# Optimization experiments

Measured on AMD Instinct MI355X. Metric: run time of the kernel, lower is better.

The kernel has to match this reference:

```python
import jax, jax.numpy as jnp
import numpy as np
import math

D_MODEL = 1024
N_HEADS = 16
D_HEAD = D_MODEL // N_HEADS

def setup_inputs() -> dict:
    key = jax.random.key(0)
    k1, k2, k3 = jax.random.split(key, 3)
    x = jax.random.normal(k1, (4, 2048, D_MODEL), dtype=jnp.float32)
    # torch Linear weights are [out, in]; kept in that layout, applied as x @ W.T
    s = 1.0 / math.sqrt(D_MODEL)
    W_qkv = jax.random.uniform(k2, (3 * D_MODEL, D_MODEL), jnp.float32, -s, s)
    W_proj = jax.random.uniform(k3, (D_MODEL, D_MODEL), jnp.float32, -s, s)
    return {"x": x, "W_qkv": W_qkv, "W_proj": W_proj}

def reference(x, W_qkv, W_proj):
    B, T, d = x.shape
    qkv = x @ W_qkv.T  # [B,T,3d]
    q, k, v = jnp.split(qkv, 3, axis=-1)
    def split(t):
        return t.reshape(B, T, N_HEADS, D_HEAD).transpose(0, 2, 1, 3)  # [B,H,T,Dh]
    q, k, v = split(q), split(k), split(v)
    scores = jnp.einsum('bhqd,bhkd->bhqk', q, k) / math.sqrt(D_HEAD)
    mask = jnp.tril(jnp.ones((T, T), dtype=bool))
    scores = jnp.where(mask, scores, -jnp.inf)
    attn = jax.nn.softmax(scores, axis=-1)
    out = jnp.einsum('bhqk,bhkd->bhqd', attn, v)  # [B,H,T,Dh]
    out = out.transpose(0, 2, 1, 3).reshape(B, T, d)
    return out @ W_proj.T
```

## Files before the change

### kernel.cpp

```cpp
#include <hip/hip_runtime.h>
#include <hip/hip_bf16.h>
#include <math.h>

typedef __attribute__((ext_vector_type(8))) short short8;
typedef __attribute__((ext_vector_type(4))) float f32x4;
typedef __attribute__((ext_vector_type(16))) float f32x16;
typedef __attribute__((ext_vector_type(2))) unsigned uint2v;
typedef __attribute__((ext_vector_type(4))) unsigned uint4v;

#define B_  4
#define T_  2048
#define DM  1024
#define NH  16
#define DH  64
#define BH  (B_*NH)
#define M_  (B_*T_)

#define QSCALE 0.18033688011112042f

static __device__ __forceinline__ short f2bf(float f) {
  unsigned u = __float_as_uint(f);
  unsigned r = (u + 0x7fff + ((u >> 16) & 1)) >> 16;
  return (short)r;
}

static __device__ __forceinline__ float bf2f(short s) {
  return __uint_as_float(((unsigned)(unsigned short)s) << 16);
}

static __device__ __forceinline__ unsigned cvtpk(float lo, float hi) {
  unsigned r;
  asm("v_cvt_pk_bf16_f32 %0, %1, %2" : "=v"(r) : "v"(lo), "v"(hi));
  return r;
}

static __device__ __forceinline__ float expasm(float x) {
  float r;
  asm("v_exp_f32 %0, %1" : "=v"(r) : "v"(x));
  return r;
}

static __device__ __forceinline__ void gload_lds16(const void* g, void* l) {
  __builtin_amdgcn_global_load_lds((const __attribute__((address_space(1))) void*)g,
                                   (__attribute__((address_space(3))) void*)l, 16, 0, 0);
}

__global__ void k_cvt3(const float4* __restrict__ x, const float4* __restrict__ wq,
                       const float4* __restrict__ wp, ushort4* __restrict__ ox,
                       ushort4* __restrict__ oq, ushort4* __restrict__ op) {
  const int n1 = M_ * DM / 4, n2 = 3 * DM * DM / 4, n3 = DM * DM / 4;
  int i = blockIdx.x * 256 + threadIdx.x;
  const float4* src;
  ushort4* dst;
  int j = i;
  if (i < n1) { src = x; dst = ox; }
  else if (i < n1 + n2) { src = wq; dst = oq; j = i - n1; }
  else if (i < n1 + n2 + n3) { src = wp; dst = op; j = i - n1 - n2; }
  else return;
  float4 v = src[j];
  ushort4 o;
  o.x = (ushort)f2bf(v.x); o.y = (ushort)f2bf(v.y);
  o.z = (ushort)f2bf(v.z); o.w = (ushort)f2bf(v.w);
  dst[j] = o;
}

#define GEMM_STAGE(SRCA, SRCB, dA, dB, m0_, n0_, k0_)                          \
  {                                                                            \
    _Pragma("unroll")                                                          \
    for (int i = 0; i < 4; ++i) {                                              \
      int lin = i * 256 + tid;                                                 \
      int row = lin >> 3, pseg = lin & 7;                                      \
      int gseg = pseg ^ (row & 7);                                             \
      gload_lds16(&SRCA[(size_t)((m0_) + row) * DM + (k0_) + gseg * 8],        \
                  &(dA)[lin * 8]);                                             \
    }                                                                          \
    _Pragma("unroll")                                                          \
    for (int i = 0; i < 4; ++i) {                                              \
      int lin = i * 256 + tid;                                                 \
      int row = lin >> 3, pseg = lin & 7;                                      \
      int gseg = pseg ^ (row & 7);                                             \
      gload_lds16(&SRCB[(size_t)((n0_) + row) * DM + (k0_) + gseg * 8],        \
                  &(dB)[lin * 8]);                                             \
    }                                                                          \
  }

#define GEMM_COMPUTE(pA, pB)                                                   \
  {                                                                            \
    _Pragma("unroll")                                                          \
    for (int kk = 0; kk < 2; ++kk) {                                           \
      short8 aF[4], bF[4];                                                     \
      _Pragma("unroll")                                                        \
      for (int m = 0; m < 4; ++m)                                              \
        aF[m] = *(const short8*)&(pA)[(wr * 64 + m * 16 + fr) * 64 +           \
                                      (((kk * 4 + fq) ^ (fr & 7)) * 8)];       \
      _Pragma("unroll")                                                        \
      for (int n = 0; n < 4; ++n)                                              \
        bF[n] = *(const short8*)&(pB)[(wc * 64 + n * 16 + fr) * 64 +           \
                                      (((kk * 4 + fq) ^ (fr & 7)) * 8)];       \
      __builtin_amdgcn_s_setprio(1);                                           \
      _Pragma("unroll")                                                        \
      for (int m = 0; m < 4; ++m)                                              \
        _Pragma("unroll")                                                      \
        for (int n = 0; n < 4; ++n)                                            \
          acc[m][n] = __builtin_amdgcn_mfma_f32_16x16x32_bf16(aF[m], bF[n],    \
                                                              acc[m][n], 0, 0, 0); \
      __builtin_amdgcn_s_setprio(0);                                           \
    }                                                                          \
  }

#define GEMM_KLOOP(SRCA, SRCB, m0_, n0_)                                       \
  GEMM_STAGE(SRCA, SRCB, sA0, sB0, m0_, n0_, 0);                               \
  {                                                                            \
    _Pragma("unroll 1")                                                        \
    for (int t = 0; t < 16; ++t) {                                             \
      short* pA = (t & 1) ? sA1 : sA0;                                         \
      short* pB = (t & 1) ? sB1 : sB0;                                         \
      if (t < 15) {                                                            \
        short* nA = (t & 1) ? sA0 : sA1;                                       \
        short* nB = (t & 1) ? sB0 : sB1;                                       \
        GEMM_STAGE(SRCA, SRCB, nA, nB, m0_, n0_, (t + 1) * 64);                \
        asm volatile("s_waitcnt vmcnt(8)" ::: "memory");                       \
      } else {                                                                 \
        asm volatile("s_waitcnt vmcnt(0)" ::: "memory");                       \
      }                                                                        \
      __builtin_amdgcn_s_barrier();                                            \
      __builtin_amdgcn_sched_barrier(0);                                       \
      GEMM_COMPUTE(pA, pB);                                                    \
      asm volatile("" ::: "memory");                                           \
      __builtin_amdgcn_s_barrier();                                            \
    }                                                                          \
  }

__global__ __launch_bounds__(256, 2) void k_gemm_qkv(
    const short* __restrict__ A,
    const short* __restrict__ W,
    short* __restrict__ Qb, short* __restrict__ Kb, short* __restrict__ Vtb) {
  const int tid = threadIdx.x;
  const int w = tid >> 6, l = tid & 63;
  const int wr = w >> 1, wc = w & 1;
  const int fq = l >> 4, fr = l & 15;
  const int m0 = blockIdx.x * 128;
  const int n0 = blockIdx.y * 128;

  __shared__ short lds[32768];
  short* sA0 = lds;
  short* sA1 = lds + 8192;
  short* sB0 = lds + 16384;
  short* sB1 = lds + 24576;

  f32x4 acc[4][4] = {};
  GEMM_KLOOP(A, W, m0, n0);
  __syncthreads();

  short* sE = lds;
  const int part = n0 >> 10;
  const int b = m0 >> 11, tloc = m0 & 2047;

  if (part < 2) {
    const float sc = part ? 1.0f : QSCALE;
#pragma unroll
    for (int m = 0; m < 4; ++m)
#pragma unroll
      for (int n = 0; n < 4; ++n)
#pragma unroll
        for (int j = 0; j < 4; ++j)
          sE[(wr * 64 + m * 16 + fq * 4 + j) * 136 + wc * 64 + n * 16 + fr] =
              f2bf(acc[m][n][j] * sc);
    __syncthreads();
    short* dst = part ? Kb : Qb;
    const int h0 = (n0 & 1023) >> 6;
#pragma unroll
    for (int v = 0; v < 8; ++v) {
      int vid = v * 256 + tid;
      int row = vid >> 4, seg = vid & 15;
      short8 val = *(const short8*)&sE[row * 136 + seg * 8];
      int h = h0 + (seg >> 3), dh0 = (seg & 7) * 8;
      *(short8*)&dst[(((size_t)(b * NH + h) * T_ + tloc + row)) * DH + dh0] = val;
    }
  } else {
#pragma unroll
    for (int m = 0; m < 4; ++m)
#pragma unroll
      for (int n = 0; n < 4; ++n) {
        uint2v pk;
        pk[0] = cvtpk(acc[m][n][0], acc[m][n][1]);
        pk[1] = cvtpk(acc[m][n][2], acc[m][n][3]);
        *(uint2v*)&sE[(wc * 64 + n * 16 + fr) * 136 + wr * 64 + m * 16 + fq * 4] = pk;
      }
    __syncthreads();
    const int h0 = (n0 & 1023) >> 6;
#pragma unroll
    for (int v = 0; v < 8; ++v) {
      int vid = v * 256 + tid;
      int col = vid >> 4, seg = vid & 15;
      short8 val = *(const short8*)&sE[col * 136 + seg * 8];
      int h = h0 + (col >> 6), dh = col & 63;
      *(short8*)&Vtb[(((size_t)(b * NH + h) * DH + dh)) * T_ + tloc + seg * 8] = val;
    }
  }
}

__global__ __launch_bounds__(256, 2) void k_gemm_proj(
    const short* __restrict__ A,
    const short* __restrict__ W,
    float* __restrict__ C) {
  const int tid = threadIdx.x;
  const int w = tid >> 6, l = tid & 63;
  const int wr = w >> 1, wc = w & 1;
  const int fq = l >> 4, fr = l & 15;
  const int m0 = blockIdx.x * 128;
  const int n0 = blockIdx.y * 128;

  __shared__ short lds[32768];
  short* sA0 = lds;
  short* sA1 = lds + 8192;
  short* sB0 = lds + 16384;
  short* sB1 = lds + 24576;

  f32x4 acc[4][4] = {};
  GEMM_KLOOP(A, W, m0, n0);

#pragma unroll
  for (int m = 0; m < 4; ++m) {
    int row0 = m0 + wr * 64 + m * 16 + fq * 4;
#pragma unroll
    for (int n = 0; n < 4; ++n) {
      int col = n0 + wc * 64 + n * 16 + fr;
#pragma unroll
      for (int j = 0; j < 4; ++j)
        C[(size_t)(row0 + j) * DM + col] = acc[m][n][j];
    }
  }
}

__global__ __launch_bounds__(256, 2) void k_attn9(
    const short* __restrict__ Qb,
    const short* __restrict__ Kb,
    const short* __restrict__ Vtb,
    short* __restrict__ Ob,
    unsigned* __restrict__ Pbuf,
    float* __restrict__ Lbuf) {
  const int tid = threadIdx.x;
  const int w = tid >> 6, l = tid & 63;
  const int lq = l & 31, hi = l >> 5;
  const int id = blockIdx.x;
  const int x = id >> 6;
  const int u = (x < 4) ? (2 * x) : (2 * (x - 4) + 1);
  const int bh = id & 63;
  const int qtA = 7 - (u >> 1);
  const int b = bh >> 4, h = bh & 15;

  __shared__ short lds[16384];
  short* sK = lds;
  short* sVt = lds + 8192;

  auto STAGE = [&](int buf, int kt) {
#pragma unroll
    for (int i = 0; i < 2; ++i) {
      int lin = i * 256 + tid;
      int row = lin >> 3, pseg = lin & 7;
      int gseg = pseg ^ (row & 7);
      gload_lds16(&Kb[((size_t)bh * T_ + kt * 64 + row) * DH + gseg * 8],
                  &sK[buf * 4096 + lin * 8]);
    }
#pragma unroll
    for (int i = 0; i < 2; ++i) {
      int lin = i * 256 + tid;
      int row = lin >> 3, pseg = lin & 7;
      int gseg = pseg ^ (row & 7);
      gload_lds16(&Vtb[((size_t)bh * DH + row) * T_ + kt * 64 + gseg * 8],
                  &sVt[buf * 4096 + lin * 8]);
    }
  };

  auto SMAX = [&](int kt, int q0s, f32x16& sa, f32x16& sb, float& lsum, short8 (&pb)[4]) {
    if (kt * 64 + 63 > q0s) {
      const int qg = q0s + lq;
#pragma unroll
      for (int r = 0; r < 16; ++r) {
        int kg0 = kt * 64 + (r & 3) + 8 * (r >> 2) + 4 * hi;
        if (kg0 > qg) sa[r] = -1e30f;
        if (kg0 + 32 > qg) sb[r] = -1e30f;
      }
    }
#pragma unroll
    for (int r = 0; r < 16; ++r) {
      sa[r] = expasm(sa[r]);
      sb[r] = expasm(sb[r]);
    }
    {
      float t[8];
#pragma unroll
      for (int i = 0; i < 8; ++i)
        t[i] = (sa[2 * i] + sa[2 * i + 1]) + (sb[2 * i] + sb[2 * i + 1]);
      float u0 = (t[0] + t[1]) + (t[2] + t[3]);
      float u1 = (t[4] + t[5]) + (t[6] + t[7]);
      lsum += u0 + u1;
    }
#pragma unroll
    for (int st = 0; st < 2; ++st) {
      const f32x16& P = st ? sb : sa;
      unsigned x0 = cvtpk(P[0], P[1]);
      unsigned x1 = cvtpk(P[2], P[3]);
      unsigned y0 = cvtpk(P[4], P[5]);
      unsigned y1 = cvtpk(P[6], P[7]);
      uint2v r0 = __builtin_amdgcn_permlane32_swap(x0, y0, false, false);
      uint2v r1 = __builtin_amdgcn_permlane32_swap(x1, y1, false, false);
      unsigned x2 = cvtpk(P[8], P[9]);
      unsigned x3 = cvtpk(P[10], P[11]);
      unsigned y2 = cvtpk(P[12], P[13]);
      unsigned y3 = cvtpk(P[14], P[15]);
      uint2v r2 = __builtin_amdgcn_permlane32_swap(x2, y2, false, false);
      uint2v r3 = __builtin_amdgcn_permlane32_swap(x3, y3, false, false);
      uint4v ta, tb;
      ta[0] = r0[0]; ta[1] = r1[0]; ta[2] = r0[1]; ta[3] = r1[1];
      tb[0] = r2[0]; tb[1] = r3[0]; tb[2] = r2[1]; tb[3] = r3[1];
      pb[st * 2 + 0] = __builtin_bit_cast(short8, ta);
      pb[st * 2 + 1] = __builtin_bit_cast(short8, tb);
    }
  };

  auto RUN_SEG = [&](int qt, int k0, int k1, int ppid) {
    const int q00 = qt * 256 + w * 32;
    const int q01 = q00 + 128;
    short8 qf0[4], qf1[4];
#pragma unroll
    for (int c = 0; c < 4; ++c) {
      qf0[c] = *(const short8*)&Qb[((size_t)bh * T_ + q00 + lq) * DH + c * 16 + hi * 8];
      qf1[c] = *(const short8*)&Qb[((size_t)bh * T_ + q01 + lq) * DH + c * 16 + hi * 8];
    }
    float ls0 = 0.f, ls1 = 0.f;
    f32x16 oa0[2] = {}, oa1[2] = {};

    auto CSUB2 = [&](int kt, const int koff) {
      const bool do0 = (kt * 64 <= q00 + 31);
      const bool do1 = (kt * 64 <= q01 + 31);
      f32x16 s0a = {}, s0b = {}, s1a = {}, s1b = {};
      __builtin_amdgcn_s_setprio(1);
#pragma unroll
      for (int st = 0; st < 2; ++st) {
        short8 kf[4];
#pragma unroll
        for (int c = 0; c < 4; ++c)
          kf[c] = *(const short8*)&sK[koff + (st * 32 + lq) * 64 +
                                      (((2 * c + hi) ^ (lq & 7)) * 8)];
        f32x16& d0 = st ? s0b : s0a;
        f32x16& d1 = st ? s1b : s1a;
#pragma unroll
        for (int c = 0; c < 4; ++c) {
          if (do0) d0 = __builtin_amdgcn_mfma_f32_32x32x16_bf16(kf[c], qf0[c], d0, 0, 0, 0);
          if (do1) d1 = __builtin_amdgcn_mfma_f32_32x32x16_bf16(kf[c], qf1[c], d1, 0, 0, 0);
        }
      }
      __builtin_amdgcn_s_setprio(0);

      short8 pb0[4], pb1[4];
      if (do0) SMAX(kt, q00, s0a, s0b, ls0, pb0);
      if (do1) SMAX(kt, q01, s1a, s1b, ls1, pb1);

      __builtin_amdgcn_s_setprio(1);
#pragma unroll
      for (int dt = 0; dt < 2; ++dt) {
        short8 vf[4];
#pragma unroll
        for (int c = 0; c < 4; ++c)
          vf[c] = *(const short8*)&sVt[koff + (dt * 32 + lq) * 64 +
                                       (((2 * c + hi) ^ (lq & 7)) * 8)];
#pragma unroll
        for (int c = 0; c < 4; ++c) {
          if (do0) oa0[dt] = __builtin_amdgcn_mfma_f32_32x32x16_bf16(vf[c], pb0[c], oa0[dt], 0, 0, 0);
          if (do1) oa1[dt] = __builtin_amdgcn_mfma_f32_32x32x16_bf16(vf[c], pb1[c], oa1[dt], 0, 0, 0);
        }
      }
      __builtin_amdgcn_s_setprio(0);
    };

    STAGE(0, k0);
    int t = k0;
    while (true) {
      if (t + 1 < k1) {
        STAGE(1, t + 1);
        asm volatile("s_waitcnt vmcnt(4)" ::: "memory");
      } else {
        asm volatile("s_waitcnt vmcnt(0)" ::: "memory");
      }
      __builtin_amdgcn_s_barrier();
      __builtin_amdgcn_sched_barrier(0);
      CSUB2(t, 0);
      __builtin_amdgcn_s_barrier();
      if (++t == k1) break;

      if (t + 1 < k1) {
        STAGE(0, t + 1);
        asm volatile("s_waitcnt vmcnt(4)" ::: "memory");
      } else {
        asm volatile("s_waitcnt vmcnt(0)" ::: "memory");
      }
      __builtin_amdgcn_s_barrier();
      __builtin_amdgcn_sched_barrier(0);
      CSUB2(t, 4096);
      __builtin_amdgcn_s_barrier();
      if (++t == k1) break;
    }

    ls0 += __shfl_xor(ls0, 32);
    ls1 += __shfl_xor(ls1, 32);

    if (ppid >= 0) {
      unsigned* Pb = Pbuf + (size_t)ppid * 8192;
#pragma unroll
      for (int sub = 0; sub < 2; ++sub) {
        const f32x16* OA = sub ? oa1 : oa0;
#pragma unroll
        for (int dt = 0; dt < 2; ++dt)
#pragma unroll
          for (int p = 0; p < 8; ++p)
            Pb[(((sub * 4 + w) * 2 + dt) * 8 + p) * 64 + l] =
                cvtpk(OA[dt][2 * p], OA[dt][2 * p + 1]);
      }
      if (hi == 0) {
        Lbuf[ppid * 256 + (0 * 4 + w) * 32 + lq] = ls0;
        Lbuf[ppid * 256 + (1 * 4 + w) * 32 + lq] = ls1;
      }
    } else {
      __syncthreads();
      short* sO = lds + w * 2304;
      const int qr = l >> 1, hf = l & 1;
      {
        float inv = 1.0f / ls0;
#pragma unroll
        for (int dt = 0; dt < 2; ++dt)
#pragma unroll
          for (int r = 0; r < 16; r += 2) {
            int dl = dt * 32 + (r & 3) + 8 * (r >> 2) + 4 * hi;
            *(unsigned*)&sO[lq * 72 + dl] = cvtpk(oa0[dt][r] * inv, oa0[dt][r + 1] * inv);
          }
        asm volatile("s_waitcnt lgkmcnt(0)" ::: "memory");
        __builtin_amdgcn_sched_barrier(0);
        const int tg = qt * 256 + w * 32 + qr;
#pragma unroll
        for (int ss = 0; ss < 4; ++ss) {
          short8 v = *(const short8*)&sO[qr * 72 + hf * 32 + ss * 8];
          *(short8*)&Ob[((size_t)(b * T_) + tg) * DM + h * 64 + hf * 32 + ss * 8] = v;
        }
        asm volatile("s_waitcnt lgkmcnt(0)" ::: "memory");
        __builtin_amdgcn_sched_barrier(0);
      }
      {
        float inv = 1.0f / ls1;
#pragma unroll
        for (int dt = 0; dt < 2; ++dt)
#pragma unroll
          for (int r = 0; r < 16; r += 2) {
            int dl = dt * 32 + (r & 3) + 8 * (r >> 2) + 4 * hi;
            *(unsigned*)&sO[lq * 72 + dl] = cvtpk(oa1[dt][r] * inv, oa1[dt][r + 1] * inv);
          }
        asm volatile("s_waitcnt lgkmcnt(0)" ::: "memory");
        __builtin_amdgcn_sched_barrier(0);
        const int tg = qt * 256 + 128 + w * 32 + qr;
#pragma unroll
        for (int ss = 0; ss < 4; ++ss) {
          short8 v = *(const short8*)&sO[qr * 72 + hf * 32 + ss * 8];
          *(short8*)&Ob[((size_t)(b * T_) + tg) * DM + h * 64 + hf * 32 + ss * 8] = v;
        }
      }
    }
  };

  if ((u & 1) == 0) {
    RUN_SEG(qtA, 0, 18, (bh * 4 + (qtA - 4)) * 2 + 0);
  } else {
    RUN_SEG(qtA, 18, 4 * qtA + 4, (bh * 4 + (qtA - 4)) * 2 + 1);
    const int qtB = u >> 1;
    RUN_SEG(qtB, 0, 4 * qtB + 4, -1);
  }
}

__global__ __launch_bounds__(256) void k_merge(
    const unsigned* __restrict__ P, const float* __restrict__ L,
    short* __restrict__ Ob) {
  const int tid = threadIdx.x;
  const int w = tid >> 6, l = tid & 63;
  const int lq = l & 31, hi = l >> 5;
  const int sid = blockIdx.x;
  const int bh = sid & 63, qtm = sid >> 6;
  const int qt = 4 + qtm;
  const int b = bh >> 4, h = bh & 15;
  const int pid0 = (bh * 4 + qtm) * 2;
  const unsigned* P0 = P + (size_t)pid0 * 8192;
  const unsigned* P1 = P0 + 8192;

  __shared__ short sOm[9216];
  short* sO = sOm + w * 2304;
  const int qr = l >> 1, hf = l & 1;

#pragma unroll
  for (int sub = 0; sub < 2; ++sub) {
    float l0 = L[pid0 * 256 + (sub * 4 + w) * 32 + lq];
    float l1 = L[(pid0 + 1) * 256 + (sub * 4 + w) * 32 + lq];
    float inv = 1.0f / (l0 + l1);
#pragma unroll
    for (int dt = 0; dt < 2; ++dt)
#pragma unroll
      for (int p = 0; p < 8; ++p) {
        int idx = (((sub * 4 + w) * 2 + dt) * 8 + p) * 64 + l;
        unsigned u0 = P0[idx], u1 = P1[idx];
        float e0 = bf2f((short)(u0 & 0xffff)) + bf2f((short)(u1 & 0xffff));
        float e1 = bf2f((short)(u0 >> 16)) + bf2f((short)(u1 >> 16));
        int r = 2 * p;
        int dl = dt * 32 + (r & 3) + 8 * (r >> 2) + 4 * hi;
        *(unsigned*)&sO[lq * 72 + dl] = cvtpk(e0 * inv, e1 * inv);
      }
    asm volatile("s_waitcnt lgkmcnt(0)" ::: "memory");
    __builtin_amdgcn_sched_barrier(0);
    const int tg = qt * 256 + sub * 128 + w * 32 + qr;
#pragma unroll
    for (int ss = 0; ss < 4; ++ss) {
      short8 v = *(const short8*)&sO[qr * 72 + hf * 32 + ss * 8];
      *(short8*)&Ob[((size_t)(b * T_) + tg) * DM + h * 64 + hf * 32 + ss * 8] = v;
    }
    asm volatile("s_waitcnt lgkmcnt(0)" ::: "memory");
    __builtin_amdgcn_sched_barrier(0);
  }
}

extern "C" void kernel_launch(void* const* d_in, const int* in_sizes, int n_in,
                              void* d_out, int out_size, void* d_ws, size_t ws_size,
                              hipStream_t stream) {
  const float* x     = (const float*)d_in[0];
  const float* Wqkv  = (const float*)d_in[1];
  const float* Wproj = (const float*)d_in[2];
  float* out = (float*)d_out;

  short* ws = (short*)d_ws;
  short* xbf   = ws;
  short* wqkvb = xbf + (size_t)M_ * DM;
  short* wprjb = wqkvb + (size_t)3 * DM * DM;
  short* Qb    = wprjb + (size_t)DM * DM;
  short* Kb    = Qb + (size_t)BH * T_ * DH;
  short* Vtb   = Kb + (size_t)BH * T_ * DH;
  short* Ob    = Vtb + (size_t)BH * T_ * DH;
  unsigned* Pbuf = (unsigned*)xbf;
  float* Lbuf    = (float*)wqkvb;

  const int ncv = (M_ * DM + 3 * DM * DM + DM * DM) / 4;
  k_cvt3<<<(ncv + 255) / 256, 256, 0, stream>>>(
      (const float4*)x, (const float4*)Wqkv, (const float4*)Wproj,
      (ushort4*)xbf, (ushort4*)wqkvb, (ushort4*)wprjb);

  k_gemm_qkv<<<dim3(M_ / 128, 3 * DM / 128), 256, 0, stream>>>(xbf, wqkvb, Qb, Kb, Vtb);
  k_attn9<<<512, 256, 0, stream>>>(Qb, Kb, Vtb, Ob, Pbuf, Lbuf);
  k_merge<<<256, 256, 0, stream>>>(Pbuf, Lbuf, Ob);
  k_gemm_proj<<<dim3(M_ / 128, DM / 128), 256, 0, stream>>>(Ob, wprjb, out);
}
```

Measured before the change: 143.5 us.

## Restructure GEMMs to 256x128 tiles with 8 waves and triple-buffered split-phase loads

Both projection GEMMs move from 128x128 tiles with 4 waves and double buffering to 256x128 tiles with 8 waves (512 threads) and a three-slot LDS ring. Each 64-wide k step is split into two phases, and each phase issues an A or B prefetch for a later stage while computing from the current slot. The aim is better B-tile reuse and more load latency hidden behind MFMA work. In exchange, each block uses 144KB of LDS, so only one block fits per CU, the grid is halved, and the epilogue indexing changes. The V-transpose epilogue now uses a 264-element LDS stride.

```diff
diff --git a/kernel.cpp b/kernel.cpp
--- a/kernel.cpp
+++ b/kernel.cpp
@@ -64,74 +64,84 @@
   dst[j] = o;
 }
 
-#define GEMM_STAGE(SRCA, SRCB, dA, dB, m0_, n0_, k0_)                          \
-  {                                                                            \
+
+#define RSLOT(s) (lds + (s) * 24576)
+
+#define R_STAGE_A(SRC, s, kt) { short* d_ = RSLOT(s);                          \
+  _Pragma("unroll")                                                            \
+  for (int i_ = 0; i_ < 4; ++i_) {                                             \
+    int lin_ = i_ * 512 + tid;                                                 \
+    int row_ = lin_ >> 3, ps_ = lin_ & 7;                                      \
+    int gs_ = ps_ ^ (row_ & 7);                                                \
+    gload_lds16(&SRC[(size_t)(m0 + row_) * DM + (kt) * 64 + gs_ * 8],          \
+                &d_[lin_ * 8]);                                                \
+  } }
+
+#define R_STAGE_B(SRC, s, kt) { short* d_ = RSLOT(s) + 16384;                  \
+  _Pragma("unroll")                                                            \
+  for (int i_ = 0; i_ < 2; ++i_) {                                             \
+    int lin_ = i_ * 512 + tid;                                                 \
+    int row_ = lin_ >> 3, ps_ = lin_ & 7;                                      \
+    int gs_ = ps_ ^ (row_ & 7);                                                \
+    gload_lds16(&SRC[(size_t)(n0 + row_) * DM + (kt) * 64 + gs_ * 8],          \
+                &d_[lin_ * 8]);                                                \
+  } }
+
+#define R_PHASE(s, kk, STAGE, WAITN) {                                         \
+  const short* pA_ = RSLOT(s);                                                 \
+  const short* pB_ = pA_ + 16384;                                              \
+  short8 aF[4], bF[4];                                                         \
+  _Pragma("unroll")                                                            \
+  for (int m_ = 0; m_ < 4; ++m_) {                                             \
+    int r_ = wr * 64 + m_ * 16 + fr;                                           \
+    aF[m_] = *(const short8*)&pA_[r_ * 64 + ((((kk) * 4 + fq) ^ (r_ & 7)) * 8)]; \
+  }                                                                            \
+  _Pragma("unroll")                                                            \
+  for (int n_ = 0; n_ < 4; ++n_) {                                             \
+    int r_ = wc * 64 + n_ * 16 + fr;                                           \
+    bF[n_] = *(const short8*)&pB_[r_ * 64 + ((((kk) * 4 + fq) ^ (r_ & 7)) * 8)]; \
+  }                                                                            \
+  STAGE;                                                                       \
+  if ((WAITN) == 6) asm volatile("s_waitcnt vmcnt(6)" ::: "memory");           \
+  else if ((WAITN) == 0) asm volatile("s_waitcnt vmcnt(0)" ::: "memory");      \
+  __builtin_amdgcn_s_barrier();                                                \
+  asm volatile("s_waitcnt lgkmcnt(0)" ::: "memory");                           \
+  __builtin_amdgcn_sched_barrier(0);                                           \
+  __builtin_amdgcn_s_setprio(1);                                               \
+  _Pragma("unroll")                                                            \
+  for (int m_ = 0; m_ < 4; ++m_)                                               \
     _Pragma("unroll")                                                          \
-    for (int i = 0; i < 4; ++i) {                                              \
-      int lin = i * 256 + tid;                                                 \
-      int row = lin >> 3, pseg = lin & 7;                                      \
-      int gseg = pseg ^ (row & 7);                                             \
-      gload_lds16(&SRCA[(size_t)((m0_) + row) * DM + (k0_) + gseg * 8],        \
-                  &(dA)[lin * 8]);                                             \
-    }                                                                          \
-    _Pragma("unroll")                                                          \
-    for (int i = 0; i < 4; ++i) {                                              \
-      int lin = i * 256 + tid;                                                 \
-      int row = lin >> 3, pseg = lin & 7;                                      \
-      int gseg = pseg ^ (row & 7);                                             \
-      gload_lds16(&SRCB[(size_t)((n0_) + row) * DM + (k0_) + gseg * 8],        \
-                  &(dB)[lin * 8]);                                             \
-    }                                                                          \
-  }
-
-#define GEMM_COMPUTE(pA, pB)                                                   \
-  {                                                                            \
-    _Pragma("unroll")                                                          \
-    for (int kk = 0; kk < 2; ++kk) {                                           \
-      short8 aF[4], bF[4];                                                     \
-      _Pragma("unroll")                                                        \
-      for (int m = 0; m < 4; ++m)                                              \
-        aF[m] = *(const short8*)&(pA)[(wr * 64 + m * 16 + fr) * 64 +           \
-                                      (((kk * 4 + fq) ^ (fr & 7)) * 8)];       \
-      _Pragma("unroll")                                                        \
-      for (int n = 0; n < 4; ++n)                                              \
-        bF[n] = *(const short8*)&(pB)[(wc * 64 + n * 16 + fr) * 64 +           \
-                                      (((kk * 4 + fq) ^ (fr & 7)) * 8)];       \
-      __builtin_amdgcn_s_setprio(1);                                           \
-      _Pragma("unroll")                                                        \
-      for (int m = 0; m < 4; ++m)                                              \
-        _Pragma("unroll")                                                      \
-        for (int n = 0; n < 4; ++n)                                            \
-          acc[m][n] = __builtin_amdgcn_mfma_f32_16x16x32_bf16(aF[m], bF[n],    \
-                                                              acc[m][n], 0, 0, 0); \
-      __builtin_amdgcn_s_setprio(0);                                           \
-    }                                                                          \
-  }
-
-#define GEMM_KLOOP(SRCA, SRCB, m0_, n0_)                                       \
-  GEMM_STAGE(SRCA, SRCB, sA0, sB0, m0_, n0_, 0);                               \
-  {                                                                            \
-    _Pragma("unroll 1")                                                        \
-    for (int t = 0; t < 16; ++t) {                                             \
-      short* pA = (t & 1) ? sA1 : sA0;                                         \
-      short* pB = (t & 1) ? sB1 : sB0;                                         \
-      if (t < 15) {                                                            \
-        short* nA = (t & 1) ? sA0 : sA1;                                       \
-        short* nB = (t & 1) ? sB0 : sB1;                                       \
-        GEMM_STAGE(SRCA, SRCB, nA, nB, m0_, n0_, (t + 1) * 64);                \
-        asm volatile("s_waitcnt vmcnt(8)" ::: "memory");                       \
-      } else {                                                                 \
-        asm volatile("s_waitcnt vmcnt(0)" ::: "memory");                       \
-      }                                                                        \
-      __builtin_amdgcn_s_barrier();                                            \
-      __builtin_amdgcn_sched_barrier(0);                                       \
-      GEMM_COMPUTE(pA, pB);                                                    \
-      asm volatile("" ::: "memory");                                           \
-      __builtin_amdgcn_s_barrier();                                            \
-    }                                                                          \
-  }
-
-__global__ __launch_bounds__(256, 2) void k_gemm_qkv(
+    for (int n_ = 0; n_ < 4; ++n_)                                             \
+      acc[m_][n_] = __builtin_amdgcn_mfma_f32_16x16x32_bf16(aF[m_], bF[n_],    \
+                                                            acc[m_][n_], 0, 0, 0); \
+  __builtin_amdgcn_s_setprio(0);                                               \
+  __builtin_amdgcn_s_barrier(); }
+
+#define R_KLOOP(SA, SB) {                                                      \
+  R_STAGE_A(SA, 0, 0); R_STAGE_B(SB, 0, 0);                                    \
+  R_STAGE_A(SA, 1, 1); R_STAGE_B(SB, 1, 1);                                    \
+  asm volatile("s_waitcnt vmcnt(6)" ::: "memory");                             \
+  __builtin_amdgcn_s_barrier();                                                \
+  _Pragma("unroll 1")                                                          \
+  for (int it_ = 0; it_ < 4; ++it_) {                                          \
+    int t0_ = 3 * it_;                                                         \
+    R_PHASE(0, 0, R_STAGE_A(SA, 2, t0_ + 2), -1)                               \
+    R_PHASE(0, 1, R_STAGE_B(SB, 2, t0_ + 2), 6)                                \
+    R_PHASE(1, 0, R_STAGE_A(SA, 0, t0_ + 3), -1)                               \
+    R_PHASE(1, 1, R_STAGE_B(SB, 0, t0_ + 3), 6)                                \
+    R_PHASE(2, 0, R_STAGE_A(SA, 1, t0_ + 4), -1)                               \
+    R_PHASE(2, 1, R_STAGE_B(SB, 1, t0_ + 4), 6)                                \
+  }                                                                            \
+  R_PHASE(0, 0, R_STAGE_A(SA, 2, 14), -1)                                      \
+  R_PHASE(0, 1, R_STAGE_B(SB, 2, 14), 6)                                       \
+  R_PHASE(1, 0, R_STAGE_A(SA, 0, 15), -1)                                      \
+  R_PHASE(1, 1, R_STAGE_B(SB, 0, 15), 6)                                       \
+  R_PHASE(2, 0, , -1)                                                          \
+  R_PHASE(2, 1, , 0)                                                           \
+  R_PHASE(0, 0, , -1)                                                          \
+  R_PHASE(0, 1, , -1) }
+
+__global__ __launch_bounds__(512) void k_gemm_qkv(
     const short* __restrict__ A,
     const short* __restrict__ W,
     short* __restrict__ Qb, short* __restrict__ Kb, short* __restrict__ Vtb) {
@@ -139,22 +149,19 @@
   const int w = tid >> 6, l = tid & 63;
   const int wr = w >> 1, wc = w & 1;
   const int fq = l >> 4, fr = l & 15;
-  const int m0 = blockIdx.x * 128;
+  const int m0 = blockIdx.x * 256;
   const int n0 = blockIdx.y * 128;
 
-  __shared__ short lds[32768];
-  short* sA0 = lds;
-  short* sA1 = lds + 8192;
-  short* sB0 = lds + 16384;
-  short* sB1 = lds + 24576;
+  __shared__ short lds[73728];
 
   f32x4 acc[4][4] = {};
-  GEMM_KLOOP(A, W, m0, n0);
+  R_KLOOP(A, W);
   __syncthreads();
 
   short* sE = lds;
   const int part = n0 >> 10;
   const int b = m0 >> 11, tloc = m0 & 2047;
+  const int h0 = (n0 & 1023) >> 6;
 
   if (part < 2) {
     const float sc = part ? 1.0f : QSCALE;
@@ -168,10 +175,9 @@
               f2bf(acc[m][n][j] * sc);
     __syncthreads();
     short* dst = part ? Kb : Qb;
-    const int h0 = (n0 & 1023) >> 6;
 #pragma unroll
     for (int v = 0; v < 8; ++v) {
-      int vid = v * 256 + tid;
+      int vid = v * 512 + tid;
       int row = vid >> 4, seg = vid & 15;
       short8 val = *(const short8*)&sE[row * 136 + seg * 8];
       int h = h0 + (seg >> 3), dh0 = (seg & 7) * 8;
@@ -185,22 +191,21 @@
         uint2v pk;
         pk[0] = cvtpk(acc[m][n][0], acc[m][n][1]);
         pk[1] = cvtpk(acc[m][n][2], acc[m][n][3]);
-        *(uint2v*)&sE[(wc * 64 + n * 16 + fr) * 136 + wr * 64 + m * 16 + fq * 4] = pk;
+        *(uint2v*)&sE[(wc * 64 + n * 16 + fr) * 264 + wr * 64 + m * 16 + fq * 4] = pk;
       }
     __syncthreads();
-    const int h0 = (n0 & 1023) >> 6;
 #pragma unroll
     for (int v = 0; v < 8; ++v) {
-      int vid = v * 256 + tid;
-      int col = vid >> 4, seg = vid & 15;
-      short8 val = *(const short8*)&sE[col * 136 + seg * 8];
+      int vid = v * 512 + tid;
+      int col = vid >> 5, seg = vid & 31;
+      short8 val = *(const short8*)&sE[col * 264 + seg * 8];
       int h = h0 + (col >> 6), dh = col & 63;
       *(short8*)&Vtb[(((size_t)(b * NH + h) * DH + dh)) * T_ + tloc + seg * 8] = val;
     }
   }
 }
 
-__global__ __launch_bounds__(256, 2) void k_gemm_proj(
+__global__ __launch_bounds__(512) void k_gemm_proj(
     const short* __restrict__ A,
     const short* __restrict__ W,
     float* __restrict__ C) {
@@ -208,17 +213,13 @@
   const int w = tid >> 6, l = tid & 63;
   const int wr = w >> 1, wc = w & 1;
   const int fq = l >> 4, fr = l & 15;
-  const int m0 = blockIdx.x * 128;
+  const int m0 = blockIdx.x * 256;
   const int n0 = blockIdx.y * 128;
 
-  __shared__ short lds[32768];
-  short* sA0 = lds;
-  short* sA1 = lds + 8192;
-  short* sB0 = lds + 16384;
-  short* sB1 = lds + 24576;
+  __shared__ short lds[73728];
 
   f32x4 acc[4][4] = {};
-  GEMM_KLOOP(A, W, m0, n0);
+  R_KLOOP(A, W);
 
 #pragma unroll
   for (int m = 0; m < 4; ++m) {
@@ -548,8 +549,8 @@
       (const float4*)x, (const float4*)Wqkv, (const float4*)Wproj,
       (ushort4*)xbf, (ushort4*)wqkvb, (ushort4*)wprjb);
 
-  k_gemm_qkv<<<dim3(M_ / 128, 3 * DM / 128), 256, 0, stream>>>(xbf, wqkvb, Qb, Kb, Vtb);
+  k_gemm_qkv<<<dim3(M_ / 256, 3 * DM / 128), 512, 0, stream>>>(xbf, wqkvb, Qb, Kb, Vtb);
   k_attn9<<<512, 256, 0, stream>>>(Qb, Kb, Vtb, Ob, Pbuf, Lbuf);
   k_merge<<<256, 256, 0, stream>>>(Pbuf, Lbuf, Ob);
-  k_gemm_proj<<<dim3(M_ / 128, DM / 128), 256, 0, stream>>>(Ob, wprjb, out);
-}
+  k_gemm_proj<<<dim3(M_ / 256, DM / 128), 512, 0, stream>>>(Ob, wprjb, out);
+}
```

Result: slower. 148.7 us (+3.6%).
